# Optimization experiments

Hardware: AMD Instinct MI355X
Metric: run time of the kernel (lower is better)

## Reference

```python
import jax, jax.numpy as jnp
import numpy as np

NUM_HEADS = 15
NUM_KV_HEADS = 5
HEAD_DIM = 64
GROUPS = NUM_HEADS // NUM_KV_HEADS
BIG_NEG = jnp.finfo(jnp.float32).min


def setup_inputs() -> dict:
    key = jax.random.key(0)
    k1, k2, k3, k4 = jax.random.split(key, 4)
    B, S = 2, 2048
    attention_mask = jax.random.randint(k1, (B, S, S), 0, 2).astype(bool)
    query_states = jax.random.normal(k2, (B, S, NUM_HEADS, HEAD_DIM), dtype=jnp.float32)
    key_states = jax.random.normal(k3, (B, S, NUM_KV_HEADS, HEAD_DIM), dtype=jnp.float32)
    value_states = jax.random.normal(k4, (B, S, NUM_KV_HEADS, HEAD_DIM), dtype=jnp.float32)
    return {
        "attention_mask": attention_mask,
        "query_states": query_states,
        "key_states": key_states,
        "value_states": value_states,
    }


def reference(attention_mask, query_states, key_states, value_states):
    B, S = query_states.shape[0], key_states.shape[1]
    # GQA: expand KV heads (each kv head repeated GROUPS times, contiguous)
    k = jnp.repeat(key_states, GROUPS, axis=2)    # [B,S,H,D]
    v = jnp.repeat(value_states, GROUPS, axis=2)  # [B,S,H,D]
    q = query_states.astype(jnp.float32)
    k = k.astype(jnp.float32)
    # scores: [B,H,Sq,Sk]
    att = jnp.einsum('bqhd,bkhd->bhqk', q, k) * (HEAD_DIM ** -0.5)
    maskf = attention_mask[:, None, :, :].astype(jnp.float32)
    att = maskf * att + (1.0 - maskf) * BIG_NEG
    probs = jax.nn.softmax(att, axis=-1).astype(v.dtype)
    # [B,H,Sq,D] -> [B,Sq,H,D] -> [B,Sq,H*D]
    out = jnp.einsum('bhqk,bkhd->bqhd', probs, v)
    return out.reshape(B, S, NUM_HEADS * HEAD_DIM)
```

## Files before the change

kernel.cpp:

```cpp
#include <hip/hip_runtime.h>
#include <hip/hip_bf16.h>

#define B_    2
#define S_    2048
#define H_    15
#define KVH_  5
#define G_    3
#define D_    64
#define KVD_  (KVH_ * D_)
#define HD_   (H_ * D_)
#define SW_   (S_ / 32)
#define KBLK  32
#define ITER  (S_ / KBLK)

constexpr float SCALE   = 0.125f;
constexpr float NEG_BIG = -3.0e38f;
constexpr float DEFER_THR = 8.0f;

typedef __bf16  bf16x8 __attribute__((ext_vector_type(8)));
typedef __bf16  bf16x4 __attribute__((ext_vector_type(4)));
typedef float   f32x4  __attribute__((ext_vector_type(4)));
typedef int     i32x4  __attribute__((ext_vector_type(4)));

#define MFMA(a, b, c) __builtin_amdgcn_mfma_f32_16x16x32_bf16((a), (b), (c), 0, 0, 0)

__device__ __forceinline__ void gload16(const void* g, void* l) {
    __builtin_amdgcn_global_load_lds(
        (const __attribute__((address_space(1))) unsigned int*)g,
        (__attribute__((address_space(3))) unsigned int*)l, 16, 0, 0);
}

__device__ __forceinline__ unsigned pack_hi16(unsigned lo_elem, unsigned hi_elem) {
    return __builtin_amdgcn_perm(hi_elem, lo_elem, 0x07060302u);
}

__global__ __launch_bounds__(256) void bitpack(const int* __restrict__ mask,
                                               unsigned int* __restrict__ bits) {
    const int i = blockIdx.x * 256 + threadIdx.x;
    unsigned long long bal = __ballot(mask[i] != 0);
    const int lane = threadIdx.x & 63;
    if (lane == 0)       bits[i >> 5] = (unsigned int)bal;
    else if (lane == 32) bits[i >> 5] = (unsigned int)(bal >> 32);
}

__global__ __launch_bounds__(256) void conv_k(const float* __restrict__ K,
                                              __bf16* __restrict__ khi,
                                              __bf16* __restrict__ klo) {
    const int i = blockIdx.x * 256 + threadIdx.x;
    const float4 v = ((const float4*)K)[i];
    const float xs[4] = {v.x, v.y, v.z, v.w};
    bf16x4 h, lo;
#pragma unroll
    for (int j = 0; j < 4; j++) {
        __bf16 hh = (__bf16)xs[j];
        h[j]  = hh;
        lo[j] = (__bf16)(xs[j] - (float)hh);
    }
    ((bf16x4*)khi)[i] = h;
    ((bf16x4*)klo)[i] = lo;
}

__global__ __launch_bounds__(256) void transpose_v(const float* __restrict__ V,
                                                   __bf16* __restrict__ vthi,
                                                   __bf16* __restrict__ vtlo) {
    __shared__ float tile[64][65];
    const int bid = blockIdx.x;
    const int st  = bid & 31;
    const int kv  = (bid >> 5) % KVH_;
    const int b   = bid / (32 * KVH_);
    const int s0  = st * 64;
    const int tid = threadIdx.x;
    const int c   = tid & 63;
    const int rq  = tid >> 6;
#pragma unroll
    for (int i = 0; i < 16; i++) {
        const int si = rq + i * 4;
        tile[si][c] = V[(((size_t)b * S_ + s0 + si) * KVH_ + kv) * D_ + c];
    }
    __syncthreads();
#pragma unroll
    for (int i = 0; i < 16; i++) {
        const int di = rq + i * 4;
        const float x = tile[c][di];
        const __bf16 hh = (__bf16)x;
        const size_t o = (((size_t)b * KVH_ + kv) * D_ + di) * S_ + s0 + c;
        vthi[o] = hh;
        vtlo[o] = (__bf16)(x - (float)hh);
    }
}

__global__ __launch_bounds__(256) void attn_main(const unsigned int* __restrict__ bits,
                                                 const float* __restrict__ Q,
                                                 const __bf16* __restrict__ khi,
                                                 const __bf16* __restrict__ klo,
                                                 const __bf16* __restrict__ vthi,
                                                 const __bf16* __restrict__ vtlo,
                                                 float* __restrict__ out) {
    __shared__ __align__(16) __bf16 Kls[2][2][KBLK][64];
    __shared__ __align__(16) __bf16 Vls[2][64][KBLK];
    __shared__ __align__(16) float  Pls[4][16][36];

    const int tid  = threadIdx.x;
    const int wv   = tid >> 6;
    const int lane = tid & 63;
    const int lrow = lane & 15;
    const int lgrp = lane >> 4;

    const int bid = blockIdx.x;
    const int qt  = bid & 31;
    const int bh  = bid >> 5;
    const int h   = bh % H_;
    const int b   = bh / H_;
    const int kv  = h / G_;
    const int q0  = qt * 64 + wv * 16;

    const float* qp = Q + (((size_t)b * S_ + (q0 + lrow)) * H_ + h) * D_;
    bf16x8 ahi[2], alo[2];
#pragma unroll
    for (int kk = 0; kk < 2; kk++) {
#pragma unroll
        for (int jj = 0; jj < 2; jj++) {
            const float4 v = *(const float4*)(qp + kk * 32 + lgrp * 8 + jj * 4);
            const float xs[4] = {v.x, v.y, v.z, v.w};
#pragma unroll
            for (int j = 0; j < 4; j++) {
                const __bf16 hh = (__bf16)xs[j];
                ahi[kk][jj * 4 + j] = hh;
                alo[kk][jj * 4 + j] = (__bf16)(xs[j] - (float)hh);
            }
        }
    }

    f32x4 O[4] = {{0.f,0.f,0.f,0.f},{0.f,0.f,0.f,0.f},{0.f,0.f,0.f,0.f},{0.f,0.f,0.f,0.f}};
    float m[4], l[4];
#pragma unroll
    for (int r = 0; r < 4; r++) { m[r] = NEG_BIG; l[r] = 0.f; }

    const __bf16* khb = khi + (size_t)b * S_ * KVD_ + kv * D_;
    const __bf16* klb = klo + (size_t)b * S_ * KVD_ + kv * D_;
    const __bf16* vhb = vthi + ((size_t)b * KVH_ + kv) * D_ * S_;
    const __bf16* vlb = vtlo + ((size_t)b * KVH_ + kv) * D_ * S_;

    const int kgi  = wv * 64 + lane;
    const int krow = kgi >> 3, kcg = kgi & 7;
    const int kcol = ((kcg ^ (krow & 7)) * 8);
    const int vrow = kgi >> 2, vcg = kgi & 3;
    const int vcol = ((vcg ^ ((vrow >> 1) & 3)) * 8);

    const __bf16* khsrc = khb + (size_t)krow * KVD_ + kcol;
    const __bf16* klsrc = klb + (size_t)krow * KVD_ + kcol;
    const __bf16* vhsrc = vhb + (size_t)vrow * S_ + vcol;
    const __bf16* vlsrc = vlb + (size_t)vrow * S_ + vcol;
    const unsigned int* bptr = bits + ((size_t)b * S_ + q0 + lgrp * 4) * SW_;

    gload16(khsrc, &Kls[0][0][wv * 8][0]);
    gload16(klsrc, &Kls[0][1][wv * 8][0]);
    khsrc += (size_t)KBLK * KVD_;
    klsrc += (size_t)KBLK * KVD_;
    __syncthreads();

    for (int kt = 0; kt < ITER; kt++) {
        const int cur = kt & 1;

        unsigned bw[4];
#pragma unroll
        for (int r = 0; r < 4; r++) bw[r] = bptr[(size_t)r * SW_];
        bptr++;

        if (kt + 1 < ITER) {
            gload16(khsrc, &Kls[cur ^ 1][0][wv * 8][0]);
            gload16(klsrc, &Kls[cur ^ 1][1][wv * 8][0]);
            khsrc += (size_t)KBLK * KVD_;
            klsrc += (size_t)KBLK * KVD_;
        }
        gload16(vhsrc, &Vls[0][wv * 16][0]);
        gload16(vlsrc, &Vls[1][wv * 16][0]);
        vhsrc += KBLK;
        vlsrc += KBLK;

        f32x4 s[2];
#pragma unroll
        for (int t = 0; t < 2; t++) {
            const int row = t * 16 + lrow;
            const int sw  = row & 7;
            const bf16x8 bh0 = *(const bf16x8*)&Kls[cur][0][row][(lgrp ^ sw) * 8];
            const bf16x8 bh1 = *(const bf16x8*)&Kls[cur][0][row][((4 + lgrp) ^ sw) * 8];
            const bf16x8 bl0 = *(const bf16x8*)&Kls[cur][1][row][(lgrp ^ sw) * 8];
            const bf16x8 bl1 = *(const bf16x8*)&Kls[cur][1][row][((4 + lgrp) ^ sw) * 8];
            f32x4 acc = {0.f, 0.f, 0.f, 0.f};
            acc = MFMA(ahi[0], bh0, acc);
            acc = MFMA(alo[0], bh0, acc);
            acc = MFMA(ahi[0], bl0, acc);
            acc = MFMA(ahi[1], bh1, acc);
            acc = MFMA(alo[1], bh1, acc);
            acc = MFMA(ahi[1], bl1, acc);
            s[t] = acc;
        }

        float tm[4];
#pragma unroll
        for (int r = 0; r < 4; r++) {
            const unsigned w = bw[r];
            const float sv0 = ((w >> lrow) & 1u)        ? s[0][r] * SCALE : NEG_BIG;
            const float sv1 = ((w >> (16 + lrow)) & 1u) ? s[1][r] * SCALE : NEG_BIG;
            s[0][r] = sv0;
            s[1][r] = sv1;
            float t = fmaxf(sv0, sv1);
            t = fmaxf(t, __shfl_xor(t, 1));
            t = fmaxf(t, __shfl_xor(t, 2));
            t = fmaxf(t, __shfl_xor(t, 4));
            t = fmaxf(t, __shfl_xor(t, 8));
            tm[r] = t;
        }

        const bool small = (tm[0] <= m[0] + DEFER_THR) && (tm[1] <= m[1] + DEFER_THR) &&
                           (tm[2] <= m[2] + DEFER_THR) && (tm[3] <= m[3] + DEFER_THR);
        if (!__all(small)) {
            float fr_[4];
#pragma unroll
            for (int r = 0; r < 4; r++) {
                const float mn = fmaxf(m[r], tm[r]);
                const float f  = __expf(m[r] - mn);
                m[r] = mn;
                l[r] *= f;
                fr_[r] = f;
            }
#pragma unroll
            for (int db = 0; db < 4; db++) {
                f32x4 o = O[db];
                o[0] *= fr_[0]; o[1] *= fr_[1]; o[2] *= fr_[2]; o[3] *= fr_[3];
                O[db] = o;
            }
        }

#pragma unroll
        for (int r = 0; r < 4; r++) {
            const float p0 = __expf(s[0][r] - m[r]);
            const float p1 = __expf(s[1][r] - m[r]);
            l[r] += p0 + p1;
            Pls[wv][lgrp * 4 + r][lrow]      = p0;
            Pls[wv][lgrp * 4 + r][16 + lrow] = p1;
        }
        __syncthreads();

        const f32x4 pa = *(const f32x4*)&Pls[wv][lrow][lgrp * 8];
        const f32x4 pb = *(const f32x4*)&Pls[wv][lrow][lgrp * 8 + 4];
        unsigned pu[8];
        float    pf[8];
#pragma unroll
        for (int j = 0; j < 4; j++) {
            pf[j]     = pa[j];
            pf[4 + j] = pb[j];
            pu[j]     = __builtin_bit_cast(unsigned, pa[j]);
            pu[4 + j] = __builtin_bit_cast(unsigned, pb[j]);
        }
        unsigned lu[8];
#pragma unroll
        for (int j = 0; j < 8; j++) {
            const float hf = __builtin_bit_cast(float, pu[j] & 0xFFFF0000u);
            lu[j] = __builtin_bit_cast(unsigned, pf[j] - hf);
        }
        i32x4 wh, wl;
#pragma unroll
        for (int i = 0; i < 4; i++) {
            wh[i] = (int)pack_hi16(pu[2 * i], pu[2 * i + 1]);
            wl[i] = (int)pack_hi16(lu[2 * i], lu[2 * i + 1]);
        }
        const bf16x8 ph = __builtin_bit_cast(bf16x8, wh);
        const bf16x8 pl = __builtin_bit_cast(bf16x8, wl);

#pragma unroll
        for (int db = 0; db < 4; db++) {
            const int row = db * 16 + lrow;
            const int sw  = (row >> 1) & 3;
            const bf16x8 vh = *(const bf16x8*)&Vls[0][row][(lgrp ^ sw) * 8];
            const bf16x8 vl = *(const bf16x8*)&Vls[1][row][(lgrp ^ sw) * 8];
            O[db] = MFMA(ph, vh, O[db]);
            O[db] = MFMA(pl, vh, O[db]);
            O[db] = MFMA(ph, vl, O[db]);
        }
        __syncthreads();
    }

#pragma unroll
    for (int r = 0; r < 4; r++) {
        float lv = l[r];
        lv += __shfl_xor(lv, 1);
        lv += __shfl_xor(lv, 2);
        lv += __shfl_xor(lv, 4);
        lv += __shfl_xor(lv, 8);
        l[r] = 1.0f / lv;
    }
#pragma unroll
    for (int db = 0; db < 4; db++) {
#pragma unroll
        for (int r = 0; r < 4; r++) {
            const int q = q0 + lgrp * 4 + r;
            out[((size_t)b * S_ + q) * HD_ + h * D_ + db * 16 + lrow] = O[db][r] * l[r];
        }
    }
}

extern "C" void kernel_launch(void* const* d_in, const int* in_sizes, int n_in,
                              void* d_out, int out_size, void* d_ws, size_t ws_size,
                              hipStream_t stream) {
    const int*   mask = (const int*)d_in[0];
    const float* Q    = (const float*)d_in[1];
    const float* K    = (const float*)d_in[2];
    const float* V    = (const float*)d_in[3];
    float*       out  = (float*)d_out;

    char* ws = (char*)d_ws;
    unsigned int* bits = (unsigned int*)ws;
    const size_t KV_BYTES = (size_t)B_ * S_ * KVH_ * D_ * sizeof(__bf16);
    __bf16* khi  = (__bf16*)(ws + (1 << 20));
    __bf16* klo  = (__bf16*)(ws + (1 << 20) + KV_BYTES);
    __bf16* vthi = (__bf16*)(ws + (1 << 20) + 2 * KV_BYTES);
    __bf16* vtlo = (__bf16*)(ws + (1 << 20) + 3 * KV_BYTES);

    bitpack<<<(B_ * S_ * S_) / 256, 256, 0, stream>>>(mask, bits);
    conv_k<<<(B_ * S_ * KVH_ * D_) / (256 * 4), 256, 0, stream>>>(K, khi, klo);
    transpose_v<<<B_ * KVH_ * (S_ / 64), 256, 0, stream>>>(V, vthi, vtlo);
    attn_main<<<B_ * H_ * (S_ / 64), 256, 0, stream>>>(bits, Q, khi, klo, vthi, vtlo, out);
}
```

Measured before the change: 261.6 us.

## Transpose MFMA operands so each lane owns one query row

Swaps the A/B operands of the QK and PV MFMAs so the score and output accumulators are laid out with one query row per lane. Row max and row sum then need only two cross-lane shuffles, and the mask needs one bit word per lane instead of four. P is packed into bf16 hi/lo words before the LDS store rather than after the load, and the output is written as float4. The softmax scale is folded into Q at load time. Together these cut shuffle count, ALU work and LDS traffic per key tile, at the cost of a reworked P shared-memory layout that must match the transposed MFMA operand mapping.

Result: faster. 245.5 us (-6.1%).

```diff
diff --git a/kernel.cpp b/kernel.cpp
--- a/kernel.cpp
+++ b/kernel.cpp
@@ -30,8 +30,8 @@
         (__attribute__((address_space(3))) unsigned int*)l, 16, 0, 0);
 }
 
-__device__ __forceinline__ unsigned pack_hi16(unsigned lo_elem, unsigned hi_elem) {
-    return __builtin_amdgcn_perm(hi_elem, lo_elem, 0x07060302u);
+__device__ __forceinline__ unsigned pack_hi16(unsigned even_elem, unsigned odd_elem) {
+    return __builtin_amdgcn_perm(odd_elem, even_elem, 0x07060302u);
 }
 
 __global__ __launch_bounds__(256) void bitpack(const int* __restrict__ mask,
@@ -96,9 +96,9 @@
                                                  const __bf16* __restrict__ vthi,
                                                  const __bf16* __restrict__ vtlo,
                                                  float* __restrict__ out) {
-    __shared__ __align__(16) __bf16 Kls[2][2][KBLK][64];
-    __shared__ __align__(16) __bf16 Vls[2][64][KBLK];
-    __shared__ __align__(16) float  Pls[4][16][36];
+    __shared__ __align__(16) __bf16   Kls[2][2][KBLK][64];
+    __shared__ __align__(16) __bf16   Vls[2][64][KBLK];
+    __shared__ __align__(16) unsigned Pw[4][2][16][20];
 
     const int tid  = threadIdx.x;
     const int wv   = tid >> 6;
@@ -121,7 +121,7 @@
 #pragma unroll
         for (int jj = 0; jj < 2; jj++) {
             const float4 v = *(const float4*)(qp + kk * 32 + lgrp * 8 + jj * 4);
-            const float xs[4] = {v.x, v.y, v.z, v.w};
+            const float xs[4] = {v.x * SCALE, v.y * SCALE, v.z * SCALE, v.w * SCALE};
 #pragma unroll
             for (int j = 0; j < 4; j++) {
                 const __bf16 hh = (__bf16)xs[j];
@@ -132,9 +132,7 @@
     }
 
     f32x4 O[4] = {{0.f,0.f,0.f,0.f},{0.f,0.f,0.f,0.f},{0.f,0.f,0.f,0.f},{0.f,0.f,0.f,0.f}};
-    float m[4], l[4];
-#pragma unroll
-    for (int r = 0; r < 4; r++) { m[r] = NEG_BIG; l[r] = 0.f; }
+    float m = NEG_BIG, l = 0.f;
 
     const __bf16* khb = khi + (size_t)b * S_ * KVD_ + kv * D_;
     const __bf16* klb = klo + (size_t)b * S_ * KVD_ + kv * D_;
@@ -151,7 +149,7 @@
     const __bf16* klsrc = klb + (size_t)krow * KVD_ + kcol;
     const __bf16* vhsrc = vhb + (size_t)vrow * S_ + vcol;
     const __bf16* vlsrc = vlb + (size_t)vrow * S_ + vcol;
-    const unsigned int* bptr = bits + ((size_t)b * S_ + q0 + lgrp * 4) * SW_;
+    const unsigned int* bptr = bits + ((size_t)b * S_ + q0 + lrow) * SW_;
 
     gload16(khsrc, &Kls[0][0][wv * 8][0]);
     gload16(klsrc, &Kls[0][1][wv * 8][0]);
@@ -162,10 +160,7 @@
     for (int kt = 0; kt < ITER; kt++) {
         const int cur = kt & 1;
 
-        unsigned bw[4];
-#pragma unroll
-        for (int r = 0; r < 4; r++) bw[r] = bptr[(size_t)r * SW_];
-        bptr++;
+        const unsigned w = *bptr++;
 
         if (kt + 1 < ITER) {
             gload16(khsrc, &Kls[cur ^ 1][0][wv * 8][0]);
@@ -188,116 +183,89 @@
             const bf16x8 bl0 = *(const bf16x8*)&Kls[cur][1][row][(lgrp ^ sw) * 8];
             const bf16x8 bl1 = *(const bf16x8*)&Kls[cur][1][row][((4 + lgrp) ^ sw) * 8];
             f32x4 acc = {0.f, 0.f, 0.f, 0.f};
-            acc = MFMA(ahi[0], bh0, acc);
-            acc = MFMA(alo[0], bh0, acc);
-            acc = MFMA(ahi[0], bl0, acc);
-            acc = MFMA(ahi[1], bh1, acc);
-            acc = MFMA(alo[1], bh1, acc);
-            acc = MFMA(ahi[1], bl1, acc);
+            acc = MFMA(bh0, ahi[0], acc);
+            acc = MFMA(bh0, alo[0], acc);
+            acc = MFMA(bl0, ahi[0], acc);
+            acc = MFMA(bh1, ahi[1], acc);
+            acc = MFMA(bh1, alo[1], acc);
+            acc = MFMA(bl1, ahi[1], acc);
             s[t] = acc;
         }
 
-        float tm[4];
-#pragma unroll
-        for (int r = 0; r < 4; r++) {
-            const unsigned w = bw[r];
-            const float sv0 = ((w >> lrow) & 1u)        ? s[0][r] * SCALE : NEG_BIG;
-            const float sv1 = ((w >> (16 + lrow)) & 1u) ? s[1][r] * SCALE : NEG_BIG;
-            s[0][r] = sv0;
-            s[1][r] = sv1;
-            float t = fmaxf(sv0, sv1);
-            t = fmaxf(t, __shfl_xor(t, 1));
-            t = fmaxf(t, __shfl_xor(t, 2));
-            t = fmaxf(t, __shfl_xor(t, 4));
-            t = fmaxf(t, __shfl_xor(t, 8));
-            tm[r] = t;
-        }
-
-        const bool small = (tm[0] <= m[0] + DEFER_THR) && (tm[1] <= m[1] + DEFER_THR) &&
-                           (tm[2] <= m[2] + DEFER_THR) && (tm[3] <= m[3] + DEFER_THR);
-        if (!__all(small)) {
-            float fr_[4];
+        float pmax = NEG_BIG;
+#pragma unroll
+        for (int t = 0; t < 2; t++) {
 #pragma unroll
             for (int r = 0; r < 4; r++) {
-                const float mn = fmaxf(m[r], tm[r]);
-                const float f  = __expf(m[r] - mn);
-                m[r] = mn;
-                l[r] *= f;
-                fr_[r] = f;
-            }
+                const int bit = t * 16 + lgrp * 4 + r;
+                const float sv = ((w >> bit) & 1u) ? s[t][r] : NEG_BIG;
+                s[t][r] = sv;
+                pmax = fmaxf(pmax, sv);
+            }
+        }
+        pmax = fmaxf(pmax, __shfl_xor(pmax, 16));
+        pmax = fmaxf(pmax, __shfl_xor(pmax, 32));
+
+        if (!__all(pmax <= m + DEFER_THR)) {
+            const float mn = fmaxf(m, pmax);
+            const float f  = __expf(m - mn);
+            m = mn;
+            l *= f;
 #pragma unroll
             for (int db = 0; db < 4; db++) {
                 f32x4 o = O[db];
-                o[0] *= fr_[0]; o[1] *= fr_[1]; o[2] *= fr_[2]; o[3] *= fr_[3];
+                o[0] *= f; o[1] *= f; o[2] *= f; o[3] *= f;
                 O[db] = o;
             }
         }
 
 #pragma unroll
-        for (int r = 0; r < 4; r++) {
-            const float p0 = __expf(s[0][r] - m[r]);
-            const float p1 = __expf(s[1][r] - m[r]);
-            l[r] += p0 + p1;
-            Pls[wv][lgrp * 4 + r][lrow]      = p0;
-            Pls[wv][lgrp * 4 + r][16 + lrow] = p1;
+        for (int t = 0; t < 2; t++) {
+            unsigned words[2][2];
+#pragma unroll
+            for (int pr = 0; pr < 2; pr++) {
+                const float e0 = __expf(s[t][2 * pr]     - m);
+                const float e1 = __expf(s[t][2 * pr + 1] - m);
+                l += e0 + e1;
+                const unsigned u0 = __builtin_bit_cast(unsigned, e0);
+                const unsigned u1 = __builtin_bit_cast(unsigned, e1);
+                const float h0 = __builtin_bit_cast(float, u0 & 0xFFFF0000u);
+                const float h1 = __builtin_bit_cast(float, u1 & 0xFFFF0000u);
+                const unsigned l0 = __builtin_bit_cast(unsigned, e0 - h0);
+                const unsigned l1 = __builtin_bit_cast(unsigned, e1 - h1);
+                words[0][pr] = pack_hi16(u0, u1);
+                words[1][pr] = pack_hi16(l0, l1);
+            }
+            *(uint2*)&Pw[wv][0][lrow][8 * t + 2 * lgrp] = make_uint2(words[0][0], words[0][1]);
+            *(uint2*)&Pw[wv][1][lrow][8 * t + 2 * lgrp] = make_uint2(words[1][0], words[1][1]);
         }
         __syncthreads();
 
-        const f32x4 pa = *(const f32x4*)&Pls[wv][lrow][lgrp * 8];
-        const f32x4 pb = *(const f32x4*)&Pls[wv][lrow][lgrp * 8 + 4];
-        unsigned pu[8];
-        float    pf[8];
-#pragma unroll
-        for (int j = 0; j < 4; j++) {
-            pf[j]     = pa[j];
-            pf[4 + j] = pb[j];
-            pu[j]     = __builtin_bit_cast(unsigned, pa[j]);
-            pu[4 + j] = __builtin_bit_cast(unsigned, pb[j]);
-        }
-        unsigned lu[8];
-#pragma unroll
-        for (int j = 0; j < 8; j++) {
-            const float hf = __builtin_bit_cast(float, pu[j] & 0xFFFF0000u);
-            lu[j] = __builtin_bit_cast(unsigned, pf[j] - hf);
-        }
-        i32x4 wh, wl;
-#pragma unroll
-        for (int i = 0; i < 4; i++) {
-            wh[i] = (int)pack_hi16(pu[2 * i], pu[2 * i + 1]);
-            wl[i] = (int)pack_hi16(lu[2 * i], lu[2 * i + 1]);
-        }
-        const bf16x8 ph = __builtin_bit_cast(bf16x8, wh);
-        const bf16x8 pl = __builtin_bit_cast(bf16x8, wl);
-
+        const bf16x8 ph = __builtin_bit_cast(bf16x8, *(const i32x4*)&Pw[wv][0][lrow][lgrp * 4]);
+        const bf16x8 pl = __builtin_bit_cast(bf16x8, *(const i32x4*)&Pw[wv][1][lrow][lgrp * 4]);
 #pragma unroll
         for (int db = 0; db < 4; db++) {
             const int row = db * 16 + lrow;
             const int sw  = (row >> 1) & 3;
             const bf16x8 vh = *(const bf16x8*)&Vls[0][row][(lgrp ^ sw) * 8];
             const bf16x8 vl = *(const bf16x8*)&Vls[1][row][(lgrp ^ sw) * 8];
-            O[db] = MFMA(ph, vh, O[db]);
-            O[db] = MFMA(pl, vh, O[db]);
-            O[db] = MFMA(ph, vl, O[db]);
+            O[db] = MFMA(vh, ph, O[db]);
+            O[db] = MFMA(vh, pl, O[db]);
+            O[db] = MFMA(vl, ph, O[db]);
         }
         __syncthreads();
     }
 
-#pragma unroll
-    for (int r = 0; r < 4; r++) {
-        float lv = l[r];
-        lv += __shfl_xor(lv, 1);
-        lv += __shfl_xor(lv, 2);
-        lv += __shfl_xor(lv, 4);
-        lv += __shfl_xor(lv, 8);
-        l[r] = 1.0f / lv;
-    }
+    float lv = l;
+    lv += __shfl_xor(lv, 16);
+    lv += __shfl_xor(lv, 32);
+    const float inv = 1.0f / lv;
+    float* op = out + ((size_t)b * S_ + q0 + lrow) * HD_ + h * D_ + lgrp * 4;
 #pragma unroll
     for (int db = 0; db < 4; db++) {
-#pragma unroll
-        for (int r = 0; r < 4; r++) {
-            const int q = q0 + lgrp * 4 + r;
-            out[((size_t)b * S_ + q) * HD_ + h * D_ + db * 16 + lrow] = O[db][r] * l[r];
-        }
+        f32x4 o = O[db];
+        o[0] *= inv; o[1] *= inv; o[2] *= inv; o[3] *= inv;
+        *(f32x4*)(op + db * 16) = o;
     }
 }
 
```
